# Kernel optimization log

Hardware: AMD Instinct MI355X
Metric: run time of the kernel (lower is better)

## Reference

```python
import jax, jax.numpy as jnp
import numpy as np

N = 100000
E = 800000
D_IN = 128
D_HID = 128
D_EMB = 128
D_OUT = 2


def setup_inputs() -> dict:
    key = jax.random.key(0)
    ks = jax.random.split(key, 16)
    x = jax.random.normal(ks[0], (N, D_IN), dtype=jnp.float32)
    edge_index = jax.random.randint(ks[1], (2, E), 0, N, dtype=jnp.int64)

    def lin(k, d_out, d_in, scale):
        return jax.random.normal(k, (d_out, d_in), dtype=jnp.float32) * scale

    s1 = 1.0 / np.sqrt(D_IN)
    s2 = 1.0 / np.sqrt(D_HID)
    s3 = 1.0 / np.sqrt(D_EMB)
    return {
        "x": x,
        "edge_index": edge_index,
        # layer 1: in -> hidden  (lin_l has bias, lin_r no bias, as in PyG SAGEConv)
        "Wl1": lin(ks[2], D_HID, D_IN, s1), "bl1": jnp.zeros((D_HID,), jnp.float32),
        "Wr1": lin(ks[3], D_HID, D_IN, s1),
        # layer 2: hidden -> hidden
        "Wl2": lin(ks[4], D_HID, D_HID, s2), "bl2": jnp.zeros((D_HID,), jnp.float32),
        "Wr2": lin(ks[5], D_HID, D_HID, s2),
        # layer 3: hidden -> embedding
        "Wl3": lin(ks[6], D_EMB, D_HID, s2), "bl3": jnp.zeros((D_EMB,), jnp.float32),
        "Wr3": lin(ks[7], D_EMB, D_HID, s2),
        # output head: embedding -> output (bias)
        "Wo": lin(ks[8], D_OUT, D_EMB, s3), "bo": jnp.zeros((D_OUT,), jnp.float32),
    }


def _sage_conv(x, src, dst, Wl, bl, Wr):
    # mean-aggregate neighbor (source) features onto destination nodes
    msg = x[src]                                             # [E, d]
    agg = jax.ops.segment_sum(msg, dst, num_segments=N)      # [N, d]
    deg = jax.ops.segment_sum(jnp.ones((src.shape[0],), x.dtype), dst, num_segments=N)
    agg = agg / jnp.maximum(deg, 1.0)[:, None]
    # out = lin_l(agg) + lin_r(x)
    return agg @ Wl.T + bl + x @ Wr.T


def reference(x, edge_index, Wl1, bl1, Wr1, Wl2, bl2, Wr2, Wl3, bl3, Wr3, Wo, bo):
    src, dst = edge_index[0], edge_index[1]
    h = jax.nn.relu(_sage_conv(x, src, dst, Wl1, bl1, Wr1))   # dropout is identity in eval
    h = jax.nn.relu(_sage_conv(h, src, dst, Wl2, bl2, Wr2))
    h = _sage_conv(h, src, dst, Wl3, bl3, Wr3)                # no relu on last conv
    return h @ Wo.T + bo                                      # [N, D_OUT]
```

## Files before the change

kernel.cpp:

```cpp
#include <hip/hip_runtime.h>
#include <stdint.h>

typedef unsigned int u32;
typedef unsigned short u16;
typedef __bf16 bf16x8 __attribute__((ext_vector_type(8)));
typedef float floatx16 __attribute__((ext_vector_type(16)));
typedef u32 u32x4 __attribute__((ext_vector_type(4)));
typedef float floatx4 __attribute__((ext_vector_type(4)));

__device__ __forceinline__ u16 f2b(float f) {
    u32 u = __builtin_bit_cast(u32, f);
    u32 r = u + 0x7FFFu + ((u >> 16) & 1u);
    return (u16)(r >> 16);
}
__device__ __forceinline__ float lo2f(u32 u) { return __builtin_bit_cast(float, u << 16); }
__device__ __forceinline__ float hi2f(u32 u) { return __builtin_bit_cast(float, u & 0xFFFF0000u); }


__device__ __forceinline__ void self_detect(const int* ei, const u32* xw, int& is64, int& isbf) {
    int lane = threadIdx.x & 63;
    int v = ei ? ei[2 * lane + 1] : 0;
    unsigned long long b1 = __ballot(v == 0);
    u32 w = xw ? xw[lane] : 0;
    u32 e = (w >> 7) & 0xFF;
    int plaus = (e == 0) || (e >= 90 && e <= 140);
    unsigned long long b2 = __ballot(plaus);
    is64 = (b1 == ~0ULL) ? 1 : 0;
    isbf = (b2 == ~0ULL) ? 1 : 0;
}

__device__ __forceinline__ int load_id(const int* __restrict__ ei, int is64, size_t pos, int N) {
    int v = is64 ? ei[2 * pos] : ei[pos];
    unsigned u = (unsigned)v;
    if (u >= (unsigned)N) u = 0;
    return (int)u;
}

__device__ __forceinline__ float load_f(const void* __restrict__ p, int isbf, size_t i) {
    if (isbf) {
        u16 s = ((const u16*)p)[i];
        return __builtin_bit_cast(float, ((u32)s) << 16);
    }
    return ((const float*)p)[i];
}


#define CH 4096
#define CAPB 3072

__global__ __launch_bounds__(1024) void front_kernel(
    const void* __restrict__ xraw, const int* __restrict__ ei, int E, int N, int cvb,
    u32* __restrict__ xb, int* __restrict__ gcur, u32* __restrict__ csrbkt,
    const void* Wl1, const void* Wr1, const void* Wl2, const void* Wr2,
    const void* Wl3, const void* Wr3, const void* b1, const void* b2,
    const void* b3, const void* Wo, const void* bo,
    u16* __restrict__ Wcp, float* __restrict__ smalls) {
    __shared__ int lhist[1024], loff[1024], lcur[1024], gofs[1024], wsum[16];
    __shared__ u32 ebuf[CH];
    __shared__ u16 ebkt[CH];
    int blk = blockIdx.x;
    int t = threadIdx.x;

    if (blk < cvb) {
        int is64, isbf;
        self_detect(nullptr, (const u32*)xraw, is64, isbf);
        int i = blk * 1024 + t;
        int count4 = N * 16;
        if (i >= count4) return;
        if (isbf) {
            ((u32x4*)xb)[i] = ((const u32x4*)xraw)[i];
        } else {
            const floatx4* f4 = (const floatx4*)xraw;
            floatx4 f0 = f4[2 * i], f1 = f4[2 * i + 1];
            u32x4 o;
            o.x = (u32)f2b(f0.x) | ((u32)f2b(f0.y) << 16);
            o.y = (u32)f2b(f0.z) | ((u32)f2b(f0.w) << 16);
            o.z = (u32)f2b(f1.x) | ((u32)f2b(f1.y) << 16);
            o.w = (u32)f2b(f1.z) | ((u32)f2b(f1.w) << 16);
            ((u32x4*)xb)[i] = o;
        }
        return;
    }
    if (blk < cvb + 12) {
        int is64, isbf;
        self_detect(nullptr, (const u32*)xraw, is64, isbf);
        int tg = (blk - cvb) * 1024 + t;
        int l = tg >> 12;
        int tt = tg & 4095;
        const void* Wl = (l == 0) ? Wl1 : (l == 1) ? Wl2 : Wl3;
        const void* Wr = (l == 0) ? Wr1 : (l == 1) ? Wr2 : Wr3;
        u16* Wout = Wcp + (size_t)l * 32768;
        int lane = tt & 63;
        int jt = (tt >> 6) & 3;
        int s = tt >> 8;
        int n = lane & 31;
        int q = lane >> 5;
        int j = jt * 32 + n;
#pragma unroll
        for (int jj = 0; jj < 8; ++jj) {
            int k = s * 16 + q * 8 + jj;
            float v = (k < 128) ? load_f(Wl, isbf, (size_t)j * 128 + k)
                                : load_f(Wr, isbf, (size_t)j * 128 + (k - 128));
            Wout[tt * 8 + jj] = f2b(v);
        }
        return;
    }
    if (blk == cvb + 12) {
        int is64, isbf;
        self_detect(nullptr, (const u32*)xraw, is64, isbf);
        if (t < 642) {
            float v;
            if (t < 128) v = load_f(b1, isbf, t);
            else if (t < 256) v = load_f(b2, isbf, t - 128);
            else if (t < 384) v = load_f(b3, isbf, t - 256);
            else if (t < 640) v = load_f(Wo, isbf, t - 384);
            else v = load_f(bo, isbf, t - 640);
            smalls[t] = v;
        }
        return;
    }

    int is64, isbf;
    self_detect(ei, nullptr, is64, isbf);
    int cbase = (blk - (cvb + 13)) * CH;
    int cn = E - cbase;
    if (cn > CH) cn = CH;
    lhist[t] = 0;
    __syncthreads();
    int mysrc[4], myb[4], mydl[4];
#pragma unroll
    for (int k = 0; k < 4; ++k) {
        int i = t + k * 1024;
        myb[k] = -1;
        if (i < cn) {
            int e = cbase + i;
            int s = load_id(ei, is64, (size_t)e, N);
            int d = load_id(ei, is64, (size_t)E + e, N);
            mysrc[k] = s;
            mydl[k] = d & 255;
            myb[k] = d >> 8;
            atomicAdd(&lhist[myb[k]], 1);
        }
    }
    __syncthreads();
    int lane = t & 63, wid = t >> 6;
    int v = lhist[t];
    int inc = v;
#pragma unroll
    for (int off = 1; off < 64; off <<= 1) {
        int o = __shfl_up(inc, off);
        if (lane >= off) inc += o;
    }
    if (lane == 63) wsum[wid] = inc;
    __syncthreads();
    int wpre = 0;
    for (int w = 0; w < wid; ++w) wpre += wsum[w];
    int excl = wpre + inc - v;
    loff[t] = excl;
    lcur[t] = excl;
    if (v > 0) gofs[t] = atomicAdd(&gcur[t], v);
    __syncthreads();
#pragma unroll
    for (int k = 0; k < 4; ++k) {
        if (myb[k] >= 0) {
            int pos = atomicAdd(&lcur[myb[k]], 1);
            ebuf[pos] = (u32)mysrc[k] | ((u32)mydl[k] << 24);
            ebkt[pos] = (u16)myb[k];
        }
    }
    __syncthreads();
#pragma unroll
    for (int k = 0; k < 4; ++k) {
        int i = t + k * 1024;
        if (i < cn) {
            int bb = ebkt[i];
            int local = gofs[bb] + (i - loff[bb]);
            if (local < CAPB) csrbkt[(size_t)bb * CAPB + local] = ebuf[i];
        }
    }
}

__global__ void csr_build_kernel(const u32* __restrict__ csrbkt, const int* __restrict__ gcur,
                                 int N, int* __restrict__ gtot,
                                 int* __restrict__ offs, int* __restrict__ cnt,
                                 int* __restrict__ csr) {
    __shared__ int lh[256], lcur[256], wsum[4];
    __shared__ int sbase;
    __shared__ u32 sbuf[CAPB];
    int t = threadIdx.x;
    int b = blockIdx.x;
    int cb = gcur[b];
    if (cb > CAPB) cb = CAPB;
    const u32* bsrc = csrbkt + (size_t)b * CAPB;
    int d0 = b << 8;
    lh[t] = 0;
    __syncthreads();
    for (int i = t; i < cb; i += 256) atomicAdd(&lh[bsrc[i] >> 24], 1);
    __syncthreads();
    int lane = t & 63, wid = t >> 6;
    int v = lh[t];
    int inc = v;
#pragma unroll
    for (int off = 1; off < 64; off <<= 1) {
        int o = __shfl_up(inc, off);
        if (lane >= off) inc += o;
    }
    if (lane == 63) wsum[wid] = inc;
    __syncthreads();
    int wpre = 0;
    for (int w = 0; w < wid; ++w) wpre += wsum[w];
    int excl = wpre + inc - v;
    lcur[t] = excl;
    if (t == 0) sbase = atomicAdd(gtot, cb);
    __syncthreads();
    int base = sbase;
    int d = d0 + t;
    if (d < N) {
        offs[d] = base + excl;
        cnt[d] = v;
    }
    for (int i = t; i < cb; i += 256) {
        u32 e = bsrc[i];
        int pos = atomicAdd(&lcur[e >> 24], 1);
        sbuf[pos] = e & 0xFFFFFFu;
    }
    __syncthreads();
    for (int i = t; i < cb; i += 256) csr[base + i] = (int)sbuf[i];
}


__global__ void agg_kernel(const u32* __restrict__ F2, const int* __restrict__ offs,
                           const int* __restrict__ cnt, const int* __restrict__ csr,
                           u32* __restrict__ Aout, int N, int E, int tstride) {
    int sub = blockIdx.x / tstride;
    int tile = blockIdx.x % tstride;
    int w = threadIdx.x >> 6;
    int lane = threadIdx.x & 63;
    int li = lane & 31;
    int half = lane >> 5;
    int nd0 = tile * 128 + sub * 16 + w * 4;
    if (nd0 >= N) return;

    int st[4], ct[4];
#pragma unroll
    for (int j = 0; j < 4; ++j) {
        int nd = nd0 + j;
        st[j] = (nd < N) ? offs[nd] : 0;
        ct[j] = (nd < N) ? cnt[nd] : 0;
    }

    float acc[4][4];
#pragma unroll
    for (int j = 0; j < 4; ++j)
#pragma unroll
        for (int f = 0; f < 4; ++f) acc[j][f] = 0.f;

    int maxct = max(max(ct[0], ct[1]), max(ct[2], ct[3]));
    int Em1 = E - 1;
    int pos = 0;
    while (pos < maxct) {
        u32 da[4][4], db[4][4];
        int vld[4][4];
#pragma unroll
        for (int j = 0; j < 4; ++j) {
#pragma unroll
            for (int k = 0; k < 4; ++k) {
                int e = pos + k * 2 + half;
                int v = (e < ct[j]) ? 1 : 0;
                vld[j][k] = v;
                int idx = st[j] + (v ? e : 0);
                if (idx > Em1) idx = Em1;
                u32 s = (u32)csr[idx] & 0xFFFFFFu;
                if (s >= (u32)N) s = 0;
                uint2 u = *reinterpret_cast<const uint2*>(F2 + ((size_t)s * 64 + li * 2));
                da[j][k] = u.x;
                db[j][k] = u.y;
            }
        }
#pragma unroll
        for (int j = 0; j < 4; ++j) {
#pragma unroll
            for (int k = 0; k < 4; ++k) {
                u32 a = vld[j][k] ? da[j][k] : 0u;
                u32 b = vld[j][k] ? db[j][k] : 0u;
                acc[j][0] += lo2f(a);
                acc[j][1] += hi2f(a);
                acc[j][2] += lo2f(b);
                acc[j][3] += hi2f(b);
            }
        }
        pos += 8;
    }

#pragma unroll
    for (int j = 0; j < 4; ++j)
#pragma unroll
        for (int f = 0; f < 4; ++f) acc[j][f] += __shfl_xor(acc[j][f], 32);

    if (half == 0) {
#pragma unroll
        for (int j = 0; j < 4; ++j) {
            int nd = nd0 + j;
            if (nd < N) {
                float sc = 1.0f / (float)(ct[j] > 1 ? ct[j] : 1);
                u32 o0 = (u32)f2b(acc[j][0] * sc) | ((u32)f2b(acc[j][1] * sc) << 16);
                u32 o1 = (u32)f2b(acc[j][2] * sc) | ((u32)f2b(acc[j][3] * sc) << 16);
                *reinterpret_cast<uint2*>(Aout + ((size_t)nd * 64 + li * 2)) =
                    make_uint2(o0, o1);
            }
        }
    }
}


__global__ void gemm_kernel(const u32* __restrict__ aggb, u32* Fio,
                            const u16* __restrict__ Wcp, const float* __restrict__ biasf,
                            int N, int relu, const float* __restrict__ headw,
                            const u32* __restrict__ xw, void* __restrict__ outp) {
    int tid = threadIdx.x;
    int w = tid >> 6;
    int lane = tid & 63;
    int nbase = blockIdx.x * 128;
    int n = lane & 31;
    int q = lane >> 5;
    int rowl = w * 32 + n;
    int node = nbase + rowl;
    int nodeC = (node < N) ? node : (N - 1);
    const u32* aRow = aggb + (size_t)nodeC * 64 + q * 4;
    const u32* fRow = Fio + (size_t)nodeC * 64 + q * 4;

    floatx16 acc0 = 0.0f, acc1 = 0.0f, acc2 = 0.0f, acc3 = 0.0f;

#pragma unroll
    for (int s = 0; s < 16; ++s) {
        const u32* ap = (s < 8) ? (aRow + (size_t)s * 8) : (fRow + (size_t)(s - 8) * 8);
        bf16x8 a = *reinterpret_cast<const bf16x8*>(ap);
        const u16* bp = Wcp + (size_t)((s * 4) * 64 + lane) * 8;
        bf16x8 b0 = *reinterpret_cast<const bf16x8*>(bp);
        bf16x8 b1 = *reinterpret_cast<const bf16x8*>(bp + 64 * 8);
        bf16x8 b2 = *reinterpret_cast<const bf16x8*>(bp + 2 * 64 * 8);
        bf16x8 b3 = *reinterpret_cast<const bf16x8*>(bp + 3 * 64 * 8);
        acc0 = __builtin_amdgcn_mfma_f32_32x32x16_bf16(a, b0, acc0, 0, 0, 0);
        acc1 = __builtin_amdgcn_mfma_f32_32x32x16_bf16(a, b1, acc1, 0, 0, 0);
        acc2 = __builtin_amdgcn_mfma_f32_32x32x16_bf16(a, b2, acc2, 0, 0, 0);
        acc3 = __builtin_amdgcn_mfma_f32_32x32x16_bf16(a, b3, acc3, 0, 0, 0);
    }

    int mbase = nbase + w * 32;
    floatx16 accs[4] = {acc0, acc1, acc2, acc3};

    if (outp == nullptr) {
#pragma unroll
        for (int jt = 0; jt < 4; ++jt) {
            int j0 = jt * 32 + n;
            float bf = biasf[j0];
#pragma unroll
            for (int r = 0; r < 16; ++r) {
                int row = (r & 3) + 8 * (r >> 2) + 4 * q;
                int nodeS = mbase + row;
                if (nodeS < N) {
                    float v = accs[jt][r] + bf;
                    if (relu) v = fmaxf(v, 0.0f);
                    u16* dst16 = (u16*)&Fio[(size_t)nodeS * 64];
                    dst16[j0] = f2b(v);
                }
            }
        }
    } else {
        int is64, isbf;
        self_detect(nullptr, xw, is64, isbf);
#pragma unroll
        for (int r = 0; r < 16; ++r) {
            float p0 = 0.f, p1 = 0.f;
#pragma unroll
            for (int jt = 0; jt < 4; ++jt) {
                int j = jt * 32 + n;
                float v = accs[jt][r] + biasf[j];
                p0 += v * headw[j];
                p1 += v * headw[128 + j];
            }
#pragma unroll
            for (int off = 16; off > 0; off >>= 1) {
                p0 += __shfl_xor(p0, off);
                p1 += __shfl_xor(p1, off);
            }
            if (n == 0) {
                int row = (r & 3) + 8 * (r >> 2) + 4 * q;
                int nodeS = mbase + row;
                if (nodeS < N) {
                    float o0 = p0 + headw[256];
                    float o1 = p1 + headw[257];
                    if (isbf)
                        ((u32*)outp)[nodeS] = (u32)f2b(o0) | ((u32)f2b(o1) << 16);
                    else
                        ((float2*)outp)[nodeS] = make_float2(o0, o1);
                }
            }
        }
    }
}

extern "C" void kernel_launch(void* const* d_in, const int* in_sizes, int n_in,
                              void* d_out, int out_size, void* d_ws, size_t ws_size,
                              hipStream_t stream) {
    const int N = in_sizes[0] / 128;
    const int E = in_sizes[1] / 2;

    const void* x = d_in[0];
    const int* ei = (const int*)d_in[1];
    const void* Wl[3] = {d_in[2], d_in[5], d_in[8]};
    const void* bl[3] = {d_in[3], d_in[6], d_in[9]};
    const void* Wr[3] = {d_in[4], d_in[7], d_in[10]};
    const void* Wo = d_in[11];
    const void* bo = d_in[12];

    char* p = (char*)d_ws;
    auto alloc = [&](size_t bytes) -> char* {
        char* r = p;
        p += (bytes + 255) & ~(size_t)255;
        return r;
    };
    int* offs = (int*)alloc((size_t)N * 4);
    int* cnt = (int*)alloc((size_t)N * 4);
    float* smalls = (float*)alloc(642 * 4);
    int* gcur = (int*)alloc(1025 * 4);
    int* csr = (int*)alloc((size_t)E * 4);
    u16* Wcp = (u16*)alloc((size_t)3 * 4096 * 8 * 2);
    u32* xb = (u32*)alloc((size_t)N * 64 * 4);
    u32* aggb = (u32*)alloc((size_t)N * 64 * 4);
    u32* csrbkt = aggb;
    int* gtot = gcur + 1024;
    (void)ws_size;

    const int NB = (N + 255) / 256;
    const int cvb = (N * 16 + 1023) / 1024;
    const int sb = (E + CH - 1) / CH;
    const int gb = (N + 127) / 128;
    const int tstride = (gb + 7) & ~7;
    const int ab = 8 * tstride;

    hipMemsetAsync(gcur, 0, 1025 * 4, stream);
    front_kernel<<<cvb + 13 + sb, 1024, 0, stream>>>(
        x, ei, E, N, cvb, xb, gcur, csrbkt,
        Wl[0], Wr[0], Wl[1], Wr[1], Wl[2], Wr[2],
        bl[0], bl[1], bl[2], Wo, bo, Wcp, smalls);
    csr_build_kernel<<<NB, 256, 0, stream>>>(csrbkt, gcur, N, gtot, offs, cnt, csr);

    agg_kernel<<<ab, 256, 0, stream>>>(xb, offs, cnt, csr, aggb, N, E, tstride);
    gemm_kernel<<<gb, 256, 0, stream>>>(aggb, xb, Wcp, smalls, N, 1, nullptr, nullptr, nullptr);
    agg_kernel<<<ab, 256, 0, stream>>>(xb, offs, cnt, csr, aggb, N, E, tstride);
    gemm_kernel<<<gb, 256, 0, stream>>>(aggb, xb, Wcp + 32768, smalls + 128, N, 1, nullptr, nullptr, nullptr);
    agg_kernel<<<ab, 256, 0, stream>>>(xb, offs, cnt, csr, aggb, N, E, tstride);
    gemm_kernel<<<gb, 256, 0, stream>>>(aggb, xb, Wcp + 65536, smalls + 256, N, 0,
                                        smalls + 384, (const u32*)x, d_out);
}
```

Before: 333.3 us.

## Fuse neighbor aggregation and GEMM into one per-layer kernel with LDS staging

Merges the separate aggregation and MFMA GEMM kernels into one layer kernel. Each block gathers mean-aggregated neighbor rows for its 128 nodes into LDS, then feeds them straight into the MFMA loop, which removes the global write and re-read of the aggregate buffer. Feature buffers now ping-pong, with a zeroed sentinel row at index N so invalid edges read zeros without branches, and the csr buffer is padded so reads past the end stay in bounds. The cost is far fewer blocks per launch (one per 128 nodes instead of eight), which lowers parallelism for the latency-bound gather, plus more LDS use per block.

```diff
diff --git a/kernel.cpp b/kernel.cpp
--- a/kernel.cpp
+++ b/kernel.cpp
@@ -15,7 +15,6 @@
 }
 __device__ __forceinline__ float lo2f(u32 u) { return __builtin_bit_cast(float, u << 16); }
 __device__ __forceinline__ float hi2f(u32 u) { return __builtin_bit_cast(float, u & 0xFFFF0000u); }
-
 
 __device__ __forceinline__ void self_detect(const int* ei, const u32* xw, int& is64, int& isbf) {
     int lane = threadIdx.x & 63;
@@ -43,7 +42,6 @@
     }
     return ((const float*)p)[i];
 }
-
 
 #define CH 4096
 #define CAPB 3072
@@ -229,112 +227,101 @@
 }
 
 
-__global__ void agg_kernel(const u32* __restrict__ F2, const int* __restrict__ offs,
-                           const int* __restrict__ cnt, const int* __restrict__ csr,
-                           u32* __restrict__ Aout, int N, int E, int tstride) {
-    int sub = blockIdx.x / tstride;
-    int tile = blockIdx.x % tstride;
-    int w = threadIdx.x >> 6;
-    int lane = threadIdx.x & 63;
+#define LSTRIDE 68
+
+__global__ __launch_bounds__(256) void layer_kernel(
+    const u32* __restrict__ xcur, u32* __restrict__ xnxt,
+    const int* __restrict__ offs, const int* __restrict__ cnt,
+    const int* __restrict__ csr,
+    const u16* __restrict__ Wcp, const float* __restrict__ biasf,
+    int N, int relu, const float* __restrict__ headw,
+    const u32* __restrict__ xw, void* __restrict__ outp) {
+    __shared__ u32 ldsA[128 * LSTRIDE];
+    int tid = threadIdx.x;
+    int w = tid >> 6;
+    int lane = tid & 63;
     int li = lane & 31;
     int half = lane >> 5;
-    int nd0 = tile * 128 + sub * 16 + w * 4;
-    if (nd0 >= N) return;
-
-    int st[4], ct[4];
-#pragma unroll
-    for (int j = 0; j < 4; ++j) {
-        int nd = nd0 + j;
-        st[j] = (nd < N) ? offs[nd] : 0;
-        ct[j] = (nd < N) ? cnt[nd] : 0;
-    }
-
-    float acc[4][4];
-#pragma unroll
-    for (int j = 0; j < 4; ++j)
-#pragma unroll
-        for (int f = 0; f < 4; ++f) acc[j][f] = 0.f;
-
-    int maxct = max(max(ct[0], ct[1]), max(ct[2], ct[3]));
-    int Em1 = E - 1;
-    int pos = 0;
-    while (pos < maxct) {
-        u32 da[4][4], db[4][4];
-        int vld[4][4];
-#pragma unroll
-        for (int j = 0; j < 4; ++j) {
-#pragma unroll
-            for (int k = 0; k < 4; ++k) {
-                int e = pos + k * 2 + half;
-                int v = (e < ct[j]) ? 1 : 0;
-                vld[j][k] = v;
-                int idx = st[j] + (v ? e : 0);
-                if (idx > Em1) idx = Em1;
-                u32 s = (u32)csr[idx] & 0xFFFFFFu;
-                if (s >= (u32)N) s = 0;
-                uint2 u = *reinterpret_cast<const uint2*>(F2 + ((size_t)s * 64 + li * 2));
-                da[j][k] = u.x;
-                db[j][k] = u.y;
-            }
-        }
-#pragma unroll
-        for (int j = 0; j < 4; ++j) {
-#pragma unroll
-            for (int k = 0; k < 4; ++k) {
-                u32 a = vld[j][k] ? da[j][k] : 0u;
-                u32 b = vld[j][k] ? db[j][k] : 0u;
-                acc[j][0] += lo2f(a);
-                acc[j][1] += hi2f(a);
-                acc[j][2] += lo2f(b);
-                acc[j][3] += hi2f(b);
-            }
-        }
-        pos += 8;
-    }
-
-#pragma unroll
-    for (int j = 0; j < 4; ++j)
-#pragma unroll
-        for (int f = 0; f < 4; ++f) acc[j][f] += __shfl_xor(acc[j][f], 32);
-
-    if (half == 0) {
+    int nbase = blockIdx.x * 128;
+    int wrow0 = w * 32;
+
+    u32 li8 = (u32)li * 8u;
+    const char* fb = (const char*)xcur;
+    for (int g = 0; g < 8; ++g) {
+        int nd0 = nbase + wrow0 + g * 4;
+        int st[4], ct[4];
 #pragma unroll
         for (int j = 0; j < 4; ++j) {
             int nd = nd0 + j;
-            if (nd < N) {
+            st[j] = (nd < N) ? offs[nd] : 0;
+            ct[j] = (nd < N) ? cnt[nd] : 0;
+        }
+        float acc[4][4];
+#pragma unroll
+        for (int j = 0; j < 4; ++j)
+#pragma unroll
+            for (int f = 0; f < 4; ++f) acc[j][f] = 0.f;
+
+        int maxct = max(max(ct[0], ct[1]), max(ct[2], ct[3]));
+        for (int pos = 0; pos < maxct; pos += 8) {
+            u32 ax[4][4], ay[4][4];
+#pragma unroll
+            for (int j = 0; j < 4; ++j) {
+                int rem = ct[j] - pos;
+                int cb = st[j] + pos + half;
+#pragma unroll
+                for (int k = 0; k < 4; ++k) {
+                    u32 sv = (u32)csr[cb + 2 * k];
+                    u32 se = ((2 * k + half) < rem) ? sv : (u32)N;
+                    u32 off = (se << 8) + li8;
+                    uint2 u = *reinterpret_cast<const uint2*>(fb + off);
+                    ax[j][k] = u.x;
+                    ay[j][k] = u.y;
+                }
+            }
+#pragma unroll
+            for (int j = 0; j < 4; ++j) {
+#pragma unroll
+                for (int k = 0; k < 4; ++k) {
+                    acc[j][0] += lo2f(ax[j][k]);
+                    acc[j][1] += hi2f(ax[j][k]);
+                    acc[j][2] += lo2f(ay[j][k]);
+                    acc[j][3] += hi2f(ay[j][k]);
+                }
+            }
+        }
+#pragma unroll
+        for (int j = 0; j < 4; ++j)
+#pragma unroll
+            for (int f = 0; f < 4; ++f) acc[j][f] += __shfl_xor(acc[j][f], 32);
+
+        if (half == 0) {
+#pragma unroll
+            for (int j = 0; j < 4; ++j) {
                 float sc = 1.0f / (float)(ct[j] > 1 ? ct[j] : 1);
                 u32 o0 = (u32)f2b(acc[j][0] * sc) | ((u32)f2b(acc[j][1] * sc) << 16);
                 u32 o1 = (u32)f2b(acc[j][2] * sc) | ((u32)f2b(acc[j][3] * sc) << 16);
-                *reinterpret_cast<uint2*>(Aout + ((size_t)nd * 64 + li * 2)) =
-                    make_uint2(o0, o1);
-            }
-        }
-    }
-}
-
-
-__global__ void gemm_kernel(const u32* __restrict__ aggb, u32* Fio,
-                            const u16* __restrict__ Wcp, const float* __restrict__ biasf,
-                            int N, int relu, const float* __restrict__ headw,
-                            const u32* __restrict__ xw, void* __restrict__ outp) {
-    int tid = threadIdx.x;
-    int w = tid >> 6;
-    int lane = tid & 63;
-    int nbase = blockIdx.x * 128;
-    int n = lane & 31;
-    int q = lane >> 5;
-    int rowl = w * 32 + n;
+                int row = wrow0 + g * 4 + j;
+                u32* lp = &ldsA[row * LSTRIDE + li * 2];
+                lp[0] = o0;
+                lp[1] = o1;
+            }
+        }
+    }
+
+    int n = li;
+    int q = half;
+    int rowl = wrow0 + n;
     int node = nbase + rowl;
     int nodeC = (node < N) ? node : (N - 1);
-    const u32* aRow = aggb + (size_t)nodeC * 64 + q * 4;
-    const u32* fRow = Fio + (size_t)nodeC * 64 + q * 4;
+    const u32* fRow = xcur + (size_t)nodeC * 64 + q * 4;
+    const u32* aRowL = &ldsA[rowl * LSTRIDE + q * 4];
 
     floatx16 acc0 = 0.0f, acc1 = 0.0f, acc2 = 0.0f, acc3 = 0.0f;
 
 #pragma unroll
-    for (int s = 0; s < 16; ++s) {
-        const u32* ap = (s < 8) ? (aRow + (size_t)s * 8) : (fRow + (size_t)(s - 8) * 8);
-        bf16x8 a = *reinterpret_cast<const bf16x8*>(ap);
+    for (int s = 0; s < 8; ++s) {
+        bf16x8 a = *reinterpret_cast<const bf16x8*>(aRowL + s * 8);
         const u16* bp = Wcp + (size_t)((s * 4) * 64 + lane) * 8;
         bf16x8 b0 = *reinterpret_cast<const bf16x8*>(bp);
         bf16x8 b1 = *reinterpret_cast<const bf16x8*>(bp + 64 * 8);
@@ -345,6 +332,19 @@
         acc2 = __builtin_amdgcn_mfma_f32_32x32x16_bf16(a, b2, acc2, 0, 0, 0);
         acc3 = __builtin_amdgcn_mfma_f32_32x32x16_bf16(a, b3, acc3, 0, 0, 0);
     }
+#pragma unroll
+    for (int s = 8; s < 16; ++s) {
+        bf16x8 a = *reinterpret_cast<const bf16x8*>(fRow + (size_t)(s - 8) * 8);
+        const u16* bp = Wcp + (size_t)((s * 4) * 64 + lane) * 8;
+        bf16x8 b0 = *reinterpret_cast<const bf16x8*>(bp);
+        bf16x8 b1 = *reinterpret_cast<const bf16x8*>(bp + 64 * 8);
+        bf16x8 b2 = *reinterpret_cast<const bf16x8*>(bp + 2 * 64 * 8);
+        bf16x8 b3 = *reinterpret_cast<const bf16x8*>(bp + 3 * 64 * 8);
+        acc0 = __builtin_amdgcn_mfma_f32_32x32x16_bf16(a, b0, acc0, 0, 0, 0);
+        acc1 = __builtin_amdgcn_mfma_f32_32x32x16_bf16(a, b1, acc1, 0, 0, 0);
+        acc2 = __builtin_amdgcn_mfma_f32_32x32x16_bf16(a, b2, acc2, 0, 0, 0);
+        acc3 = __builtin_amdgcn_mfma_f32_32x32x16_bf16(a, b3, acc3, 0, 0, 0);
+    }
 
     int mbase = nbase + w * 32;
     floatx16 accs[4] = {acc0, acc1, acc2, acc3};
@@ -361,7 +361,7 @@
                 if (nodeS < N) {
                     float v = accs[jt][r] + bf;
                     if (relu) v = fmaxf(v, 0.0f);
-                    u16* dst16 = (u16*)&Fio[(size_t)nodeS * 64];
+                    u16* dst16 = (u16*)&xnxt[(size_t)nodeS * 64];
                     dst16[j0] = f2b(v);
                 }
             }
@@ -424,11 +424,11 @@
     int* cnt = (int*)alloc((size_t)N * 4);
     float* smalls = (float*)alloc(642 * 4);
     int* gcur = (int*)alloc(1025 * 4);
-    int* csr = (int*)alloc((size_t)E * 4);
+    int* csr = (int*)alloc(((size_t)E + CAPB + 64) * 4);
     u16* Wcp = (u16*)alloc((size_t)3 * 4096 * 8 * 2);
-    u32* xb = (u32*)alloc((size_t)N * 64 * 4);
-    u32* aggb = (u32*)alloc((size_t)N * 64 * 4);
-    u32* csrbkt = aggb;
+    u32* x0 = (u32*)alloc((size_t)(N + 1) * 64 * 4);
+    u32* x1 = (u32*)alloc((size_t)(N + 1) * 64 * 4);
+    u32* csrbkt = x1;
     int* gtot = gcur + 1024;
     (void)ws_size;
 
@@ -436,21 +436,20 @@
     const int cvb = (N * 16 + 1023) / 1024;
     const int sb = (E + CH - 1) / CH;
     const int gb = (N + 127) / 128;
-    const int tstride = (gb + 7) & ~7;
-    const int ab = 8 * tstride;
 
     hipMemsetAsync(gcur, 0, 1025 * 4, stream);
     front_kernel<<<cvb + 13 + sb, 1024, 0, stream>>>(
-        x, ei, E, N, cvb, xb, gcur, csrbkt,
+        x, ei, E, N, cvb, x0, gcur, csrbkt,
         Wl[0], Wr[0], Wl[1], Wr[1], Wl[2], Wr[2],
         bl[0], bl[1], bl[2], Wo, bo, Wcp, smalls);
     csr_build_kernel<<<NB, 256, 0, stream>>>(csrbkt, gcur, N, gtot, offs, cnt, csr);
-
-    agg_kernel<<<ab, 256, 0, stream>>>(xb, offs, cnt, csr, aggb, N, E, tstride);
-    gemm_kernel<<<gb, 256, 0, stream>>>(aggb, xb, Wcp, smalls, N, 1, nullptr, nullptr, nullptr);
-    agg_kernel<<<ab, 256, 0, stream>>>(xb, offs, cnt, csr, aggb, N, E, tstride);
-    gemm_kernel<<<gb, 256, 0, stream>>>(aggb, xb, Wcp + 32768, smalls + 128, N, 1, nullptr, nullptr, nullptr);
-    agg_kernel<<<ab, 256, 0, stream>>>(xb, offs, cnt, csr, aggb, N, E, tstride);
-    gemm_kernel<<<gb, 256, 0, stream>>>(aggb, xb, Wcp + 65536, smalls + 256, N, 0,
-                                        smalls + 384, (const u32*)x, d_out);
-}
+    hipMemsetAsync(x0 + (size_t)N * 64, 0, 256, stream);
+    hipMemsetAsync(x1 + (size_t)N * 64, 0, 256, stream);
+
+    layer_kernel<<<gb, 256, 0, stream>>>(x0, x1, offs, cnt, csr, Wcp, smalls, N, 1,
+                                         nullptr, nullptr, nullptr);
+    layer_kernel<<<gb, 256, 0, stream>>>(x1, x0, offs, cnt, csr, Wcp + 32768, smalls + 128, N, 1,
+                                         nullptr, nullptr, nullptr);
+    layer_kernel<<<gb, 256, 0, stream>>>(x0, x1, offs, cnt, csr, Wcp + 65536, smalls + 256, N, 0,
+                                         smalls + 384, (const u32*)x, d_out);
+}
```

Measured after the change: 390.5 us. 17.2% more time.
